# Kernel tuning notes

Hardware: AMD Instinct MI355X
Metric: run time of the kernel (lower is better)

The kernel has to match this reference:

```python
import jax, jax.numpy as jnp
import numpy as np

DIN = 1024
DIM = 1024
NUM_HEADS = 16
HEAD_DIM = DIM // NUM_HEADS
SEQ_LEN = 2048
BATCH = 2


def setup_inputs() -> dict:
    key = jax.random.key(0)
    ks = jax.random.split(key, 5)
    s = 0.02
    x = jax.random.normal(ks[0], (BATCH, SEQ_LEN, DIN), dtype=jnp.float32)
    # torch nn.Linear weights are (out_features, in_features)
    wq = jax.random.normal(ks[1], (DIM, DIN), dtype=jnp.float32) * s
    wk = jax.random.normal(ks[2], (DIM, DIN), dtype=jnp.float32) * s
    wv = jax.random.normal(ks[3], (DIM, DIN), dtype=jnp.float32) * s
    wo = jax.random.normal(ks[4], (DIM, DIM), dtype=jnp.float32) * s
    return {"x": x, "wq": wq, "wk": wk, "wv": wv, "wo": wo}


def reference(x, wq, wk, wv, wo):
    bs, seq_len, _ = x.shape
    # project and split heads: [b, h, s, d]
    def split(z):
        return z.reshape(bs, seq_len, NUM_HEADS, HEAD_DIM).transpose(0, 2, 1, 3)
    q = split(x @ wq.T)
    k = split(x @ wk.T)
    v = split(x @ wv.T)
    # raw scores, causal mask applied BEFORE the 1/sqrt(d) scaling (as in source;
    # -inf is invariant to positive scaling so math matches standard causal attn)
    att = jnp.einsum('bhqd,bhkd->bhqk', q, k)
    causal = jnp.triu(jnp.ones((seq_len, seq_len), dtype=bool), k=1)
    att = jnp.where(causal, -jnp.inf, att)
    att = jax.nn.softmax(att / jnp.sqrt(jnp.float32(HEAD_DIM)), axis=-1)
    ctx = jnp.einsum('bhqk,bhkd->bhqd', att, v)
    ctx = ctx.transpose(0, 2, 1, 3).reshape(bs, seq_len, DIM)
    return ctx @ wo.T
```

## Files before the change

kernel.cpp:

```cpp
#include <hip/hip_runtime.h>
#include <stdint.h>

#define DIN 1024
#define DIMM 1024
#define NH 16
#define HD 64
#define SEQ 2048
#define BATCH 2
#define MTOT (BATCH*SEQ)
#define SCALE 0.125f

typedef __bf16 bf16;
typedef __bf16 bf16x8 __attribute__((ext_vector_type(8)));
typedef __bf16 bf16x4 __attribute__((ext_vector_type(4)));
typedef float f32x4 __attribute__((ext_vector_type(4)));

__device__ __forceinline__ void async16(bf16* lds, const bf16* g) {
  __builtin_amdgcn_global_load_lds(
      (const __attribute__((address_space(1))) void*)g,
      (__attribute__((address_space(3))) void*)lds, 16, 0, 0);
}

#define WAIT_VM(n)  asm volatile("s_waitcnt vmcnt(" #n ")" ::: "memory")
#define BARRIER()   asm volatile("s_barrier" ::: "memory")

__global__ __launch_bounds__(256) void convert_all(const float* __restrict__ x,
                                                   const float* __restrict__ wq,
                                                   const float* __restrict__ wk,
                                                   const float* __restrict__ wv,
                                                   const float* __restrict__ wo,
                                                   bf16* __restrict__ xb,
                                                   bf16* __restrict__ Wb) {
  const int t = blockIdx.x * 256 + threadIdx.x;
#pragma unroll
  for (int i = 0; i < 4; ++i) {
    const int c = t + i * 262144;
    const float* src;
    bf16* dst;
    if (c < 524288) {
      src = x + (size_t)c * 8;
      dst = xb + (size_t)c * 8;
    } else {
      const int cw = c - 524288;
      const int w = cw >> 17;
      const int off = (cw & 131071) * 8;
      const float* wp = (w == 0) ? wq : (w == 1) ? wk : (w == 2) ? wv : wo;
      src = wp + off;
      dst = Wb + (size_t)w * 1048576 + off;
    }
    f32x4 a = *(const f32x4*)src;
    f32x4 b = *(const f32x4*)(src + 4);
    bf16x8 r;
    r[0] = (bf16)a[0]; r[1] = (bf16)a[1]; r[2] = (bf16)a[2]; r[3] = (bf16)a[3];
    r[4] = (bf16)b[0]; r[5] = (bf16)b[1]; r[6] = (bf16)b[2]; r[7] = (bf16)b[3];
    *(bf16x8*)dst = r;
  }
}

__global__ __launch_bounds__(256, 2) void qkv_gemm(const bf16* __restrict__ A,
                                                   const bf16* __restrict__ B,
                                                   bf16* __restrict__ Q,
                                                   bf16* __restrict__ Kb,
                                                   bf16* __restrict__ Vt) {
  __shared__ bf16 As0[128 * 64];
  __shared__ bf16 As1[128 * 64];
  __shared__ bf16 Bs0[192 * 64];
  __shared__ bf16 Bs1[192 * 64];
  const int tid  = threadIdx.x;
  const int lane = tid & 63;
  const int wave = tid >> 6;
  const int lrow = lane & 15;
  const int quad = lane >> 4;
  const int wrow = wave >> 1;
  const int wcol = wave & 1;
  const int lin  = blockIdx.x;
  const int xcd  = lin & 7;
  const int idx  = lin >> 3;
  const int nbase = (xcd * 2 + (idx & 1)) * 192;
  const int mbase = (idx >> 1) * 128;

  const int srow = tid >> 3;
  const int sdst = srow * 64 + (tid & 7) * 8;
  const int sx   = ((tid & 7) ^ (srow & 7)) * 8;

  const bf16* ap = A + (size_t)(mbase + srow) * DIN + sx;
  const bf16* bp = B + (size_t)(nbase + srow) * DIN + sx;

  f32x4 acc[4][6] = {};

#define QKV_STAGE(Asb, Bsb)                                          \
  do {                                                               \
    _Pragma("unroll")                                                \
    for (int i = 0; i < 4; ++i)                                      \
      async16(&Asb[sdst + i * 2048], ap + (size_t)i * 32 * DIN);     \
    _Pragma("unroll")                                                \
    for (int i = 0; i < 6; ++i)                                      \
      async16(&Bsb[sdst + i * 2048], bp + (size_t)i * 32 * DIN);     \
  } while (0)

#define QKV_COMPUTE(Asb, Bsb)                                        \
  do {                                                               \
    __builtin_amdgcn_s_setprio(1);                                   \
    _Pragma("unroll")                                                \
    for (int h = 0; h < 2; ++h) {                                    \
      const int cx = ((h * 4 + quad) ^ (lrow & 7)) * 8;              \
      bf16x8 af[4], bfr[6];                                          \
      _Pragma("unroll")                                              \
      for (int i = 0; i < 4; ++i)                                    \
        af[i] = *(const bf16x8*)&Asb[(wrow * 64 + i * 16 + lrow) * 64 + cx]; \
      _Pragma("unroll")                                              \
      for (int j = 0; j < 6; ++j)                                    \
        bfr[j] = *(const bf16x8*)&Bsb[(wcol * 96 + j * 16 + lrow) * 64 + cx]; \
      _Pragma("unroll")                                              \
      for (int i = 0; i < 4; ++i)                                    \
        _Pragma("unroll")                                            \
        for (int j = 0; j < 6; ++j)                                  \
          acc[i][j] = __builtin_amdgcn_mfma_f32_16x16x32_bf16(af[i], bfr[j], acc[i][j], 0, 0, 0); \
    }                                                                \
    __builtin_amdgcn_s_setprio(0);                                   \
  } while (0)

  QKV_STAGE(As0, Bs0);
  WAIT_VM(0);
  BARRIER();

#pragma unroll 1
  for (int t = 0; t < 16; t += 2) {
    ap += 64; bp += 64;
    QKV_STAGE(As1, Bs1);
    WAIT_VM(10);
    BARRIER();
    QKV_COMPUTE(As0, Bs0);
    BARRIER();
    if (t + 2 < 16) {
      ap += 64; bp += 64;
      QKV_STAGE(As0, Bs0);
      WAIT_VM(10);
    } else {
      WAIT_VM(0);
    }
    BARRIER();
    QKV_COMPUTE(As1, Bs1);
    BARRIER();
  }

#undef QKV_STAGE
#undef QKV_COMPUTE

  const float C1 = 0.18033688f;
#pragma unroll
  for (int mt = 0; mt < 4; ++mt) {
    const int m0 = mbase + wrow * 64 + mt * 16 + quad * 4;
#pragma unroll
    for (int nt = 0; nt < 6; ++nt) {
      const int n16 = nbase + wcol * 96 + nt * 16;
      const int n = n16 + lrow;
      if (n16 < 1024) {
#pragma unroll
        for (int rr = 0; rr < 4; ++rr)
          Q[(size_t)(m0 + rr) * 1024 + n] = (bf16)(acc[mt][nt][rr] * C1);
      } else if (n16 < 2048) {
#pragma unroll
        for (int rr = 0; rr < 4; ++rr)
          Kb[(size_t)(m0 + rr) * 1024 + (n - 1024)] = (bf16)acc[mt][nt][rr];
      } else {
        const int nn = n - 2048;
        const int row = ((m0 >> 11) * 16 + (nn >> 6)) * 64 + (nn & 63);
        bf16x4 ov;
#pragma unroll
        for (int rr = 0; rr < 4; ++rr) ov[rr] = (bf16)acc[mt][nt][rr];
        *(bf16x4*)&Vt[(size_t)row * SEQ + (m0 & 2047)] = ov;
      }
    }
  }
}

__global__ __launch_bounds__(256, 2) void proj_gemm(const bf16* __restrict__ A,
                                                    const bf16* __restrict__ B,
                                                    float* __restrict__ C) {
  __shared__ bf16 As0[128 * 64];
  __shared__ bf16 As1[128 * 64];
  __shared__ bf16 Bs0[64 * 64];
  __shared__ bf16 Bs1[64 * 64];
  const int tid  = threadIdx.x;
  const int lane = tid & 63;
  const int wave = tid >> 6;
  const int lrow = lane & 15;
  const int quad = lane >> 4;
  const int wr = (wave >> 1) * 64;
  const int wc = (wave & 1) * 32;
  const int lin = blockIdx.x;
  const int xcd = lin & 7;
  const int idx = lin >> 3;
  const int nbase = (xcd * 2 + (idx & 1)) * 64;
  const int mbase = (idx >> 1) * 128;
  const int srow = tid >> 3;
  const int sdst = srow * 64 + (tid & 7) * 8;
  const int sx   = ((tid & 7) ^ (srow & 7)) * 8;

  const bf16* ap = A + (size_t)(mbase + srow) * DIMM + sx;
  const bf16* bp = B + (size_t)(nbase + srow) * DIMM + sx;

  f32x4 acc[4][2] = {};

#define PRJ_STAGE(Asb, Bsb)                                          \
  do {                                                               \
    _Pragma("unroll")                                                \
    for (int i = 0; i < 4; ++i)                                      \
      async16(&Asb[sdst + i * 2048], ap + (size_t)i * 32 * DIMM);    \
    _Pragma("unroll")                                                \
    for (int i = 0; i < 2; ++i)                                      \
      async16(&Bsb[sdst + i * 2048], bp + (size_t)i * 32 * DIMM);    \
  } while (0)

#define PRJ_COMPUTE(Asb, Bsb)                                        \
  do {                                                               \
    __builtin_amdgcn_s_setprio(1);                                   \
    _Pragma("unroll")                                                \
    for (int h = 0; h < 2; ++h) {                                    \
      const int cx = ((h * 4 + quad) ^ (lrow & 7)) * 8;              \
      bf16x8 af[4], bfr[2];                                          \
      _Pragma("unroll")                                              \
      for (int i = 0; i < 4; ++i)                                    \
        af[i] = *(const bf16x8*)&Asb[(wr + i * 16 + lrow) * 64 + cx]; \
      _Pragma("unroll")                                              \
      for (int i = 0; i < 2; ++i)                                    \
        bfr[i] = *(const bf16x8*)&Bsb[(wc + i * 16 + lrow) * 64 + cx]; \
      _Pragma("unroll")                                              \
      for (int mt = 0; mt < 4; ++mt)                                 \
        _Pragma("unroll")                                            \
        for (int nt = 0; nt < 2; ++nt)                               \
          acc[mt][nt] = __builtin_amdgcn_mfma_f32_16x16x32_bf16(af[mt], bfr[nt], acc[mt][nt], 0, 0, 0); \
    }                                                                \
    __builtin_amdgcn_s_setprio(0);                                   \
  } while (0)

  PRJ_STAGE(As0, Bs0);
  WAIT_VM(0);
  BARRIER();

#pragma unroll 1
  for (int t = 0; t < 16; t += 2) {
    ap += 64; bp += 64;
    PRJ_STAGE(As1, Bs1);
    WAIT_VM(6);
    BARRIER();
    PRJ_COMPUTE(As0, Bs0);
    BARRIER();
    if (t + 2 < 16) {
      ap += 64; bp += 64;
      PRJ_STAGE(As0, Bs0);
      WAIT_VM(6);
    } else {
      WAIT_VM(0);
    }
    BARRIER();
    PRJ_COMPUTE(As1, Bs1);
    BARRIER();
  }

#undef PRJ_STAGE
#undef PRJ_COMPUTE

#pragma unroll
  for (int mt = 0; mt < 4; ++mt) {
    const int m0 = mbase + wr + mt * 16 + quad * 4;
#pragma unroll
    for (int nt = 0; nt < 2; ++nt) {
      const int n = nbase + wc + nt * 16 + lrow;
#pragma unroll
      for (int rr = 0; rr < 4; ++rr)
        C[(size_t)(m0 + rr) * 1024 + n] = acc[mt][nt][rr];
    }
  }
}

__global__ __launch_bounds__(256, 2) void attn(const bf16* __restrict__ Q,
                                               const bf16* __restrict__ K,
                                               const bf16* __restrict__ Vt,
                                               bf16* __restrict__ O) {
  __shared__ bf16 Ks[2][128 * 64];
  __shared__ bf16 Vts[2][128 * 64];
  const int tid  = threadIdx.x;
  const int wave = tid >> 6;
  const int lane = tid & 63;
  const int lrow = lane & 15;
  const int quad = lane >> 4;
  const int lin  = blockIdx.x;
  const int bh   = lin & 31;
  const int pp   = lin >> 5;
  const int b = bh >> 4;
  const int h = bh & 15;

  const bf16* Qh  = Q  + (size_t)(b * SEQ) * DIMM + h * HD;
  const bf16* Kh  = K  + (size_t)(b * SEQ) * DIMM + h * HD;
  const bf16* Vth = Vt + (size_t)bh * 64 * SEQ;

  const int srow = tid >> 3;
  const int sdst = srow * 64 + (tid & 7) * 8;
  const int sx   = ((tid & 7) ^ (srow & 7)) * 8;
  const int cx0 = ((0 + quad) ^ (lrow & 7)) * 8;
  const int cx1 = ((4 + quad) ^ (lrow & 7)) * 8;
  const int LL = lrow & 7;
  const int qh = quad >> 1, ql = quad & 1;
  int vc[4];
#pragma unroll
  for (int g = 0; g < 4; ++g)
    vc[g] = ((((2 * g + qh) ^ LL) << 1) | ql) * 4;

#define ATT_STAGE(buf, kg, vg)                                        \
  do {                                                                \
    _Pragma("unroll")                                                 \
    for (int i = 0; i < 4; ++i)                                       \
      async16(&Ks[buf][sdst + i * 2048], kg + (size_t)i * 32 * DIMM); \
    async16(&Vts[buf][sdst],        vg);                              \
    async16(&Vts[buf][sdst + 2048], vg + (size_t)32 * SEQ);           \
    async16(&Vts[buf][sdst + 4096], vg + 64);                         \
    async16(&Vts[buf][sdst + 6144], vg + (size_t)32 * SEQ + 64);      \
  } while (0)

#pragma unroll 1
  for (int seg = 0; seg < 2; ++seg) {
    const int qi = seg ? pp : (31 - pp);
    const int qw = qi * 64 + wave * 16;
    const int nt = (qi + 2) >> 1;

    bf16x8 qf0 = *(const bf16x8*)&Qh[(size_t)(qw + lrow) * DIMM + quad * 8];
    bf16x8 qf1 = *(const bf16x8*)&Qh[(size_t)(qw + lrow) * DIMM + 32 + quad * 8];

    const bf16* kg = Kh + (size_t)srow * DIMM + sx;
    const bf16* vg = Vth + (size_t)srow * SEQ + sx;

    ATT_STAGE(0, kg, vg);
    __syncthreads();

    f32x4 lacc = {};
    f32x4 o_acc[4] = {};
    int cur = 0;

    for (int kt = 0; kt < nt; ++kt) {
      if (kt + 1 < nt) {
        kg += 128 * DIMM; vg += 128;
        const int nb = cur ^ 1;
        ATT_STAGE(nb, kg, vg);
      }
      const bf16* Kc = Ks[cur];
      const bf16* Vc = Vts[cur];
      f32x4 s[8];
#pragma unroll
      for (int gg = 0; gg < 8; ++gg) {
        s[gg] = f32x4{};
        bf16x8 kf0 = *(const bf16x8*)&Kc[(gg * 16 + lrow) * 64 + cx0];
        bf16x8 kf1 = *(const bf16x8*)&Kc[(gg * 16 + lrow) * 64 + cx1];
        s[gg] = __builtin_amdgcn_mfma_f32_16x16x32_bf16(kf0, qf0, s[gg], 0, 0, 0);
        s[gg] = __builtin_amdgcn_mfma_f32_16x16x32_bf16(kf1, qf1, s[gg], 0, 0, 0);
      }
      if (kt == nt - 1) {
        const int qrow = qw + lrow;
        const int kbase = kt * 128;
#pragma unroll
        for (int gg = 0; gg < 8; ++gg)
#pragma unroll
          for (int r = 0; r < 4; ++r)
            s[gg][r] = (kbase + gg * 16 + quad * 4 + r > qrow) ? -1e30f : s[gg][r];
      }
      bf16x8 pf0, pf1, pf2, pf3;
#pragma unroll
      for (int gg = 0; gg < 8; ++gg)
#pragma unroll
        for (int r = 0; r < 4; ++r) {
          const float p = __builtin_amdgcn_exp2f(s[gg][r]);
          lacc[r] += p;
          if      (gg < 2) pf0[(gg & 1) * 4 + r] = (bf16)p;
          else if (gg < 4) pf1[(gg & 1) * 4 + r] = (bf16)p;
          else if (gg < 6) pf2[(gg & 1) * 4 + r] = (bf16)p;
          else             pf3[(gg & 1) * 4 + r] = (bf16)p;
        }
#pragma unroll
      for (int dt = 0; dt < 4; ++dt) {
        const bf16* Vr0 = &Vc[(dt * 16 + lrow) * 64];
        const bf16* Vr1 = &Vc[4096 + (dt * 16 + lrow) * 64];
        bf16x4 a0 = *(const bf16x4*)&Vr0[vc[0]];
        bf16x4 a1 = *(const bf16x4*)&Vr0[vc[1]];
        bf16x4 b0 = *(const bf16x4*)&Vr0[vc[2]];
        bf16x4 b1 = *(const bf16x4*)&Vr0[vc[3]];
        bf16x4 c0 = *(const bf16x4*)&Vr1[vc[0]];
        bf16x4 c1 = *(const bf16x4*)&Vr1[vc[1]];
        bf16x4 d0 = *(const bf16x4*)&Vr1[vc[2]];
        bf16x4 d1 = *(const bf16x4*)&Vr1[vc[3]];
        bf16x8 vA = __builtin_shufflevector(a0, a1, 0, 1, 2, 3, 4, 5, 6, 7);
        bf16x8 vB = __builtin_shufflevector(b0, b1, 0, 1, 2, 3, 4, 5, 6, 7);
        bf16x8 vC = __builtin_shufflevector(c0, c1, 0, 1, 2, 3, 4, 5, 6, 7);
        bf16x8 vD = __builtin_shufflevector(d0, d1, 0, 1, 2, 3, 4, 5, 6, 7);
        o_acc[dt] = __builtin_amdgcn_mfma_f32_16x16x32_bf16(vA, pf0, o_acc[dt], 0, 0, 0);
        o_acc[dt] = __builtin_amdgcn_mfma_f32_16x16x32_bf16(vB, pf1, o_acc[dt], 0, 0, 0);
        o_acc[dt] = __builtin_amdgcn_mfma_f32_16x16x32_bf16(vC, pf2, o_acc[dt], 0, 0, 0);
        o_acc[dt] = __builtin_amdgcn_mfma_f32_16x16x32_bf16(vD, pf3, o_acc[dt], 0, 0, 0);
      }
      __syncthreads();
      cur ^= 1;
    }

    float lsum = (lacc[0] + lacc[1]) + (lacc[2] + lacc[3]);
    lsum += __shfl_xor(lsum, 16);
    lsum += __shfl_xor(lsum, 32);
    const float rl = __builtin_amdgcn_rcpf(lsum);
    bf16* Ob = O + (size_t)(b * SEQ + qw + lrow) * DIMM + h * HD;
#pragma unroll
    for (int dt = 0; dt < 4; ++dt) {
      bf16x4 ov;
#pragma unroll
      for (int r = 0; r < 4; ++r)
        ov[r] = (bf16)(o_acc[dt][r] * rl);
      *(bf16x4*)&Ob[dt * 16 + quad * 4] = ov;
    }
  }
#undef ATT_STAGE
}

extern "C" void kernel_launch(void* const* d_in, const int* in_sizes, int n_in,
                              void* d_out, int out_size, void* d_ws, size_t ws_size,
                              hipStream_t stream) {
  const float* x  = (const float*)d_in[0];
  const float* wq = (const float*)d_in[1];
  const float* wk = (const float*)d_in[2];
  const float* wv = (const float*)d_in[3];
  const float* wo = (const float*)d_in[4];

  const size_t M4 = (size_t)MTOT * DIMM;
  bf16* xb  = (bf16*)d_ws;
  bf16* Wb  = xb + M4;
  bf16* Q   = Wb + M4;
  bf16* Kb  = Q + M4;
  bf16* Vt  = Kb + M4;
  bf16* CTX = xb;
  float* out = (float*)d_out;

  convert_all<<<dim3(1024), dim3(256), 0, stream>>>(x, wq, wk, wv, wo, xb, Wb);
  qkv_gemm<<<dim3(512), dim3(256), 0, stream>>>(xb, Wb, Q, Kb, Vt);
  attn<<<dim3(512), dim3(256), 0, stream>>>(Q, Kb, Vt, CTX);
  proj_gemm<<<dim3(512), dim3(256), 0, stream>>>(CTX, Wb + 3 * 1048576, out);
}
```

Before: 162.6 us.

## Enlarge QKV GEMM tile to 256x192 with 8 waves and interleaved loads

The QKV projection GEMM now uses 512-thread blocks that each compute a 256x192 output tile, halving the grid to 256 blocks. This doubles reuse of each B tile across more rows of A. The main loop is restructured so that async global-to-LDS loads for the next stage are spread across four MFMA sub-phases, separated by extra barriers. In exchange it uses more LDS per block, adds more barriers per iteration, and with 256 blocks on the device there may be fewer blocks resident per CU.

Measured after the change: 163.6 us. Within noise of the previous version (+0.6%).

```diff
diff --git a/kernel.cpp b/kernel.cpp
--- a/kernel.cpp
+++ b/kernel.cpp
@@ -57,13 +57,13 @@
   }
 }
 
-__global__ __launch_bounds__(256, 2) void qkv_gemm(const bf16* __restrict__ A,
+__global__ __launch_bounds__(512, 2) void qkv_gemm(const bf16* __restrict__ A,
                                                    const bf16* __restrict__ B,
                                                    bf16* __restrict__ Q,
                                                    bf16* __restrict__ Kb,
                                                    bf16* __restrict__ Vt) {
-  __shared__ bf16 As0[128 * 64];
-  __shared__ bf16 As1[128 * 64];
+  __shared__ bf16 As0[256 * 64];
+  __shared__ bf16 As1[256 * 64];
   __shared__ bf16 Bs0[192 * 64];
   __shared__ bf16 Bs1[192 * 64];
   const int tid  = threadIdx.x;
@@ -71,13 +71,13 @@
   const int wave = tid >> 6;
   const int lrow = lane & 15;
   const int quad = lane >> 4;
-  const int wrow = wave >> 1;
-  const int wcol = wave & 1;
+  const int wm   = wave >> 1;
+  const int wn   = wave & 1;
   const int lin  = blockIdx.x;
   const int xcd  = lin & 7;
   const int idx  = lin >> 3;
   const int nbase = (xcd * 2 + (idx & 1)) * 192;
-  const int mbase = (idx >> 1) * 128;
+  const int mbase = (idx >> 1) * 256;
 
   const int srow = tid >> 3;
   const int sdst = srow * 64 + (tid & 7) * 8;
@@ -87,73 +87,107 @@
   const bf16* bp = B + (size_t)(nbase + srow) * DIN + sx;
 
   f32x4 acc[4][6] = {};
-
-#define QKV_STAGE(Asb, Bsb)                                          \
-  do {                                                               \
-    _Pragma("unroll")                                                \
-    for (int i = 0; i < 4; ++i)                                      \
-      async16(&Asb[sdst + i * 2048], ap + (size_t)i * 32 * DIN);     \
-    _Pragma("unroll")                                                \
-    for (int i = 0; i < 6; ++i)                                      \
-      async16(&Bsb[sdst + i * 2048], bp + (size_t)i * 32 * DIN);     \
+  const int aRow = wm * 64;
+  const int bRow = wn * 96;
+  const int cxa = (quad ^ (lrow & 7)) * 8;
+  const int cxb = ((4 + quad) ^ (lrow & 7)) * 8;
+
+#define MFMA12(AF, BQ, J0)                                               \
+  do {                                                                   \
+    __builtin_amdgcn_s_setprio(1);                                       \
+    _Pragma("unroll")                                                    \
+    for (int i = 0; i < 4; ++i)                                          \
+      _Pragma("unroll")                                                  \
+      for (int j = 0; j < 3; ++j)                                        \
+        acc[i][J0 + j] = __builtin_amdgcn_mfma_f32_16x16x32_bf16(        \
+            AF[i], BQ[j], acc[i][J0 + j], 0, 0, 0);                      \
+    __builtin_amdgcn_s_setprio(0);                                       \
   } while (0)
 
-#define QKV_COMPUTE(Asb, Bsb)                                        \
-  do {                                                               \
-    __builtin_amdgcn_s_setprio(1);                                   \
-    _Pragma("unroll")                                                \
-    for (int h = 0; h < 2; ++h) {                                    \
-      const int cx = ((h * 4 + quad) ^ (lrow & 7)) * 8;              \
-      bf16x8 af[4], bfr[6];                                          \
-      _Pragma("unroll")                                              \
-      for (int i = 0; i < 4; ++i)                                    \
-        af[i] = *(const bf16x8*)&Asb[(wrow * 64 + i * 16 + lrow) * 64 + cx]; \
-      _Pragma("unroll")                                              \
-      for (int j = 0; j < 6; ++j)                                    \
-        bfr[j] = *(const bf16x8*)&Bsb[(wcol * 96 + j * 16 + lrow) * 64 + cx]; \
-      _Pragma("unroll")                                              \
-      for (int i = 0; i < 4; ++i)                                    \
-        _Pragma("unroll")                                            \
-        for (int j = 0; j < 6; ++j)                                  \
-          acc[i][j] = __builtin_amdgcn_mfma_f32_16x16x32_bf16(af[i], bfr[j], acc[i][j], 0, 0, 0); \
-    }                                                                \
-    __builtin_amdgcn_s_setprio(0);                                   \
+#define QKV_TILE(AsC, BsC, AsN, BsN, ISSUE)                              \
+  do {                                                                   \
+             \
+    if (ISSUE) {                                                         \
+      bp += 64;                                                          \
+      async16(&BsN[sdst], bp);                              \
+      WAIT_VM(1);                                                        \
+    } else {                                                             \
+      WAIT_VM(0);                                                        \
+    }                                                                    \
+    BARRIER();                 \
+    bf16x8 af[4], bq[3];                                                 \
+                                        \
+    _Pragma("unroll")                                                    \
+    for (int i = 0; i < 4; ++i)                                          \
+      af[i] = *(const bf16x8*)&AsC[(aRow + i * 16 + lrow) * 64 + cxa];   \
+    _Pragma("unroll")                                                    \
+    for (int j = 0; j < 3; ++j)                                          \
+      bq[j] = *(const bf16x8*)&BsC[(bRow + j * 16 + lrow) * 64 + cxa];   \
+    if (ISSUE) {                                                         \
+      async16(&BsN[sdst + 4096], bp + (size_t)64 * DIN);                 \
+      async16(&BsN[sdst + 8192], bp + (size_t)128 * DIN);                \
+    }                                                                    \
+    BARRIER();                                                           \
+    MFMA12(af, bq, 0);                                                   \
+    BARRIER();                                                           \
+                            \
+    _Pragma("unroll")                                                    \
+    for (int j = 0; j < 3; ++j)                                          \
+      bq[j] = *(const bf16x8*)&BsC[(bRow + (3 + j) * 16 + lrow) * 64 + cxa]; \
+    if (ISSUE) {                                                         \
+      ap += 64;                                                          \
+      async16(&AsN[sdst],        ap);                                    \
+      async16(&AsN[sdst + 4096], ap + (size_t)64 * DIN);                 \
+    }                                                                    \
+    BARRIER();                                                           \
+    MFMA12(af, bq, 3);                                                   \
+    BARRIER();                                                           \
+                                        \
+    _Pragma("unroll")                                                    \
+    for (int i = 0; i < 4; ++i)                                          \
+      af[i] = *(const bf16x8*)&AsC[(aRow + i * 16 + lrow) * 64 + cxb];   \
+    _Pragma("unroll")                                                    \
+    for (int j = 0; j < 3; ++j)                                          \
+      bq[j] = *(const bf16x8*)&BsC[(bRow + j * 16 + lrow) * 64 + cxb];   \
+    if (ISSUE) {                                                         \
+      async16(&AsN[sdst + 8192],  ap + (size_t)128 * DIN);               \
+      async16(&AsN[sdst + 12288], ap + (size_t)192 * DIN);               \
+    }                                                                    \
+    BARRIER();                                                           \
+    MFMA12(af, bq, 0);                                                   \
+    BARRIER();                                                           \
+                                        \
+    _Pragma("unroll")                                                    \
+    for (int j = 0; j < 3; ++j)                                          \
+      bq[j] = *(const bf16x8*)&BsC[(bRow + (3 + j) * 16 + lrow) * 64 + cxb]; \
+    BARRIER();                                                           \
+    MFMA12(af, bq, 3);                                                   \
+    BARRIER();    \
   } while (0)
 
-  QKV_STAGE(As0, Bs0);
-  WAIT_VM(0);
-  BARRIER();
+#pragma unroll
+  for (int i = 0; i < 3; ++i)
+    async16(&Bs0[sdst + i * 4096], bp + (size_t)i * 64 * DIN);
+#pragma unroll
+  for (int i = 0; i < 4; ++i)
+    async16(&As0[sdst + i * 4096], ap + (size_t)i * 64 * DIN);
 
 #pragma unroll 1
   for (int t = 0; t < 16; t += 2) {
-    ap += 64; bp += 64;
-    QKV_STAGE(As1, Bs1);
-    WAIT_VM(10);
-    BARRIER();
-    QKV_COMPUTE(As0, Bs0);
-    BARRIER();
-    if (t + 2 < 16) {
-      ap += 64; bp += 64;
-      QKV_STAGE(As0, Bs0);
-      WAIT_VM(10);
-    } else {
-      WAIT_VM(0);
-    }
-    BARRIER();
-    QKV_COMPUTE(As1, Bs1);
-    BARRIER();
-  }
-
-#undef QKV_STAGE
-#undef QKV_COMPUTE
+    QKV_TILE(As0, Bs0, As1, Bs1, true);
+    QKV_TILE(As1, Bs1, As0, Bs0, (t + 2 < 16));
+  }
+
+#undef QKV_TILE
+#undef MFMA12
 
   const float C1 = 0.18033688f;
 #pragma unroll
   for (int mt = 0; mt < 4; ++mt) {
-    const int m0 = mbase + wrow * 64 + mt * 16 + quad * 4;
+    const int m0 = mbase + wm * 64 + mt * 16 + quad * 4;
 #pragma unroll
     for (int nt = 0; nt < 6; ++nt) {
-      const int n16 = nbase + wcol * 96 + nt * 16;
+      const int n16 = nbase + wn * 96 + nt * 16;
       const int n = n16 + lrow;
       if (n16 < 1024) {
 #pragma unroll
@@ -437,7 +471,7 @@
   float* out = (float*)d_out;
 
   convert_all<<<dim3(1024), dim3(256), 0, stream>>>(x, wq, wk, wv, wo, xb, Wb);
-  qkv_gemm<<<dim3(512), dim3(256), 0, stream>>>(xb, Wb, Q, Kb, Vt);
+  qkv_gemm<<<dim3(256), dim3(512), 0, stream>>>(xb, Wb, Q, Kb, Vt);
   attn<<<dim3(512), dim3(256), 0, stream>>>(Q, Kb, Vt, CTX);
   proj_gemm<<<dim3(512), dim3(256), 0, stream>>>(CTX, Wb + 3 * 1048576, out);
 }
```
